# Kernel optimization log

Measured on AMD Instinct MI355X. Metric: run time of the kernel, lower is better.

The kernel has to match this reference:

```python
import jax, jax.numpy as jnp
import numpy as np

N, LQ, D_MODEL, M_HEADS, P_POINTS, H_DIM, W_DIM = 8, 4096, 256, 8, 4, 64, 64


def setup_inputs() -> dict:
    key = jax.random.key(0)
    ks = jax.random.split(key, 9)
    d = D_MODEL
    scale = 1.0 / np.sqrt(d).astype(np.float32)
    return {
        "query": jax.random.normal(ks[0], (N, LQ, d), jnp.float32),
        "reference_points": jax.random.uniform(ks[1], (N, LQ, 2), jnp.float32),
        "input_flatten": jax.random.normal(ks[2], (N, H_DIM * W_DIM, d), jnp.float32),
        "H": H_DIM,
        "W": W_DIM,
        "Wv": jax.random.normal(ks[3], (d, d), jnp.float32) * scale,
        "bv": jnp.zeros((d,), jnp.float32),
        "Woff": jax.random.normal(ks[4], (M_HEADS * P_POINTS * 2, d), jnp.float32) * 0.01,
        "boff": jax.random.normal(ks[5], (M_HEADS * P_POINTS * 2,), jnp.float32) * 0.5,
        "Wa": jax.random.normal(ks[6], (M_HEADS * P_POINTS, d), jnp.float32) * 0.01,
        "ba": jnp.zeros((M_HEADS * P_POINTS,), jnp.float32),
        "Wo": jax.random.normal(ks[7], (d, d), jnp.float32) * scale,
        "bo": jnp.zeros((d,), jnp.float32),
    }


def _bilinear_sample(val, grid, H, W):
    # val: [B, D, H*W]; grid: [B, Lq, P, 2] in [-1, 1] (x, y); align_corners=False, zero padding.
    B, D, _ = val.shape
    _, Lq, P, _ = grid.shape
    x = (grid[..., 0] + 1.0) * (W * 0.5) - 0.5
    y = (grid[..., 1] + 1.0) * (H * 0.5) - 0.5
    x0 = jnp.floor(x)
    y0 = jnp.floor(y)
    x0i = x0.astype(jnp.int32)
    y0i = y0.astype(jnp.int32)
    wx1 = x - x0
    wy1 = y - y0
    out = jnp.zeros((B, D, Lq, P), val.dtype)
    for xi, wx in ((x0i, 1.0 - wx1), (x0i + 1, wx1)):
        for yi, wy in ((y0i, 1.0 - wy1), (y0i + 1, wy1)):
            valid = (xi >= 0) & (xi < W) & (yi >= 0) & (yi < H)
            idx = jnp.clip(yi, 0, H - 1) * W + jnp.clip(xi, 0, W - 1)  # [B, Lq, P]
            g = jnp.take_along_axis(val, idx.reshape(B, 1, Lq * P), axis=2).reshape(B, D, Lq, P)
            w = jnp.where(valid, wx * wy, 0.0)
            out = out + g * w[:, None]
    return out


def reference(query, reference_points, input_flatten, H, W, Wv, bv, Woff, boff, Wa, ba, Wo, bo):
    n, lq, d = query.shape
    m, p = M_HEADS, P_POINTS
    dh = d // m
    value = (input_flatten @ Wv.T + bv).reshape(n, H * W, m, dh)
    offsets = (query @ Woff.T + boff).reshape(n, lq, m, p, 2)
    attw = jax.nn.softmax((query @ Wa.T + ba).reshape(n, lq, m, p), axis=-1)
    normalizer = jnp.array([W, H], dtype=query.dtype)  # [W, H] order per torch code
    loc = reference_points[:, :, None, None, :] + offsets / normalizer
    grid = 2.0 * loc - 1.0  # [n, lq, m, p, 2]
    # value -> [n*m, dh, H*W] matching torch flatten(2).transpose(1,2).reshape
    val = jnp.transpose(value, (0, 2, 3, 1)).reshape(n * m, dh, H * W)
    grd = jnp.transpose(grid, (0, 2, 1, 3, 4)).reshape(n * m, lq, p, 2)
    samp = _bilinear_sample(val, grd, H, W)  # [n*m, dh, lq, p]
    aw = jnp.transpose(attw, (0, 2, 1, 3)).reshape(n * m, 1, lq, p)
    out = (samp * aw).sum(-1).reshape(n, m * dh, lq)
    out = jnp.transpose(out, (0, 2, 1))  # [n, lq, d]
    return out @ Wo.T + bo
```

## Files before the change

### kernel.cpp

```cpp
#include <hip/hip_runtime.h>
#include <math.h>

#define NB   8
#define LQN  4096
#define DM   256
#define MH   8
#define PP   4
#define HH   64
#define WW   64
#define PW   67
#define PPIX (PW*PW)

typedef __bf16 bf16x8 __attribute__((ext_vector_type(8)));
typedef float  f32x4  __attribute__((ext_vector_type(4)));
typedef unsigned short us8 __attribute__((ext_vector_type(8)));
typedef unsigned short us4 __attribute__((ext_vector_type(4)));

__device__ __forceinline__ unsigned short f2bf(float f) {
    unsigned u = __float_as_uint(f);
    u += 0x7FFFu + ((u >> 16) & 1u);
    return (unsigned short)(u >> 16);
}
__device__ __forceinline__ float bf2f(unsigned short b) {
    return __uint_as_float((unsigned)b << 16);
}

__device__ __forceinline__ void gl2lds16(const void* g, unsigned short* l) {
    __builtin_amdgcn_global_load_lds(
        (const __attribute__((address_space(1))) void*)g,
        (__attribute__((address_space(3))) void*)l,
        16, 0, 0);
}

__device__ __forceinline__ bf16x8 cvt_frag(const unsigned short* s, int row, int kq) {
    const int u0 = row * 8 + ((kq * 2) ^ (row & 7));
    const int u1 = u0 ^ 1;
    const f32x4 a0 = *(const f32x4*)&s[u0 * 8];
    const f32x4 a1 = *(const f32x4*)&s[u1 * 8];
    bf16x8 v;
    v[0] = (__bf16)a0[0]; v[1] = (__bf16)a0[1];
    v[2] = (__bf16)a0[2]; v[3] = (__bf16)a0[3];
    v[4] = (__bf16)a1[0]; v[5] = (__bf16)a1[1];
    v[6] = (__bf16)a1[2]; v[7] = (__bf16)a1[3];
    return v;
}

__global__ __launch_bounds__(256)
void prep_kernel(const float* __restrict__ Wv, const float* __restrict__ Wo,
                 const float* __restrict__ Woff, const float* __restrict__ Wa,
                 const float* __restrict__ boff, const float* __restrict__ ba,
                 unsigned short* __restrict__ Wvh, unsigned short* __restrict__ Woh,
                 unsigned short* __restrict__ Wcath, float* __restrict__ bcat,
                 unsigned short* __restrict__ valueP) {
    const int i = blockIdx.x * 256 + threadIdx.x;
    if (i < 65536) {
        Wvh[i] = f2bf(Wv[i]);
    } else if (i < 131072) {
        const int j = i - 65536;
        Woh[j] = f2bf(Wo[j]);
    } else if (i < 163840) {
        const int j = i - 131072, n = j >> 8, k = j & 255;
        const float v = (n < 64) ? Woff[n * 256 + k]
                                 : ((n < 96) ? Wa[(n - 64) * 256 + k] : 0.f);
        Wcath[j] = f2bf(v);
    } else if (i < 163968) {
        const int n = i - 163840;
        bcat[n] = (n < 64) ? boff[n] : ((n < 96) ? ba[n - 64] : 0.f);
    } else if (i < 163968 + 201216) {
        const int j   = i - 163968;
        const int c4  = j & 63;
        const int pix = j >> 6;
        const int n   = pix / 393;
        const int r   = pix - n * 393;
        int x, y;
        if (r < 201) {
            const int q = r / 67;
            y = (q == 0) ? 0 : (q == 1 ? 65 : 66);
            x = r - q * 67;
        } else {
            const int q = r - 201;
            y = 1 + q / 3;
            const int s = q - (q / 3) * 3;
            x = (s == 0) ? 0 : (s == 1 ? 65 : 66);
        }
        const size_t addr = ((size_t)n * PPIX + (size_t)y * PW + x) * DM + c4 * 4;
        *(ushort4*)&valueP[addr] = make_ushort4(0, 0, 0, 0);
    }
}

__global__ __launch_bounds__(256, 4)
void value_gemm(const float* __restrict__ Ain,
                const unsigned short* __restrict__ Wvh,
                const float* __restrict__ bv,
                unsigned short* __restrict__ valueP) {
    constexpr int K = 256, NK = 8;
    __shared__ unsigned short sA[2][4096];
    __shared__ unsigned short sB[2][4096];

    const int t   = threadIdx.x;
    const int blk = blockIdx.x;
    const int xb  = blk & 7;
    const int idx = blk >> 3;
    const int brow = xb * 4096 + (idx >> 1) * 64;
    const int bcol = (idx & 1) * 128;

    const int srow = t >> 3;
    const int scq  = (t & 7) ^ (srow & 7);
    const float* aG = Ain + (size_t)(brow + srow) * K + scq * 4;
    const size_t aI = (size_t)32 * K;

    const unsigned short* bG = Wvh + (size_t)(bcol + (t >> 2)) * K + (t & 3) * 8;
    const size_t bI = (size_t)64 * K;

    const int l   = t & 63;
    const int wid = t >> 6;
    const int wr  = wid >> 1, wc = wid & 1;
    const int fr  = l & 15,   kq = l >> 4;

    f32x4 acc[2][4] = {};

#define STAGE(buf, ks_) { const int k0_ = (ks_) * 32;                    \
       gl2lds16(aG + k0_,      &sA[buf][t * 8]);                         \
       gl2lds16(aG + k0_ + aI, &sA[buf][2048 + t * 8]);                  \
       gl2lds16(bG + k0_,      &sB[buf][t * 8]);                         \
       gl2lds16(bG + k0_ + bI, &sB[buf][2048 + t * 8]); }

    STAGE(0, 0);
    STAGE(1, 1);

    for (int ks = 0; ks < NK; ++ks) {
        const int cur = ks & 1;
        if (ks < NK - 1) asm volatile("s_waitcnt vmcnt(4)" ::: "memory");
        else             asm volatile("s_waitcnt vmcnt(0)" ::: "memory");
        __builtin_amdgcn_s_barrier();
        __builtin_amdgcn_sched_barrier(0);

        bf16x8 af[2], bf_[4];
#pragma unroll
        for (int m = 0; m < 2; ++m)
            af[m]  = cvt_frag(sA[cur], wr * 32 + m * 16 + fr, kq);
#pragma unroll
        for (int n = 0; n < 4; ++n)
            bf_[n] = *(const bf16x8*)&sB[cur][(wc * 64 + n * 16 + fr) * 32 + kq * 8];

        __builtin_amdgcn_s_setprio(1);
#pragma unroll
        for (int m = 0; m < 2; ++m)
#pragma unroll
            for (int n = 0; n < 4; ++n)
                acc[m][n] = __builtin_amdgcn_mfma_f32_16x16x32_bf16(
                    bf_[n], af[m], acc[m][n], 0, 0, 0);
        __builtin_amdgcn_s_setprio(0);

        __builtin_amdgcn_sched_barrier(0);
        __builtin_amdgcn_s_barrier();
        if (ks + 2 < NK) STAGE(cur, ks + 2);
    }
#undef STAGE

#pragma unroll
    for (int m = 0; m < 2; ++m) {
        const int row = brow + wr * 32 + m * 16 + fr;
        const int nb_ = row >> 12;
        const int pix = row & 4095;
        const int y   = pix >> 6, x = pix & 63;
        const size_t rbase =
            ((size_t)nb_ * PPIX + (size_t)(y + 1) * PW + (x + 1)) * DM;
#pragma unroll
        for (int n = 0; n < 4; ++n) {
            const int colq = bcol + wc * 64 + n * 16 + kq * 4;
            const float4 b4 = *(const float4*)&bv[colq];
            us4 o;
            o[0] = f2bf(acc[m][n][0] + b4.x);
            o[1] = f2bf(acc[m][n][1] + b4.y);
            o[2] = f2bf(acc[m][n][2] + b4.z);
            o[3] = f2bf(acc[m][n][3] + b4.w);
            *(us4*)&valueP[rbase + colq] = o;
        }
    }
}

__global__ __launch_bounds__(512, 4)
void fused_lso(const float* __restrict__ query, const float* __restrict__ refp,
               const unsigned short* __restrict__ valueP,
               const unsigned short* __restrict__ Wcath,
               const float* __restrict__ bcat,
               const unsigned short* __restrict__ Woh,
               const float* __restrict__ bo, float* __restrict__ C) {
    constexpr int K = 256, NK = 8;
    extern __shared__ unsigned short smem[];
    unsigned short* sS = smem;
    unsigned short* sB = smem + 16384;
    unsigned short* sL = smem + 32768;

    const int t    = threadIdx.x;
    const int blk  = blockIdx.x;
    const int nb   = blk & 7;
    const int brow = nb * 4096 + (blk >> 3) * 64;
    const int w    = t >> 6;
    const int lane = t & 63;
    const int fr   = lane & 15, kq = lane >> 4;

    {
        unsigned short* sQ = sS;
        unsigned short* sW = sS + 8192;

        const int srow = t >> 3;
        const int scq  = (t & 7) ^ (srow & 7);
        const float* aG = query + (size_t)(brow + srow) * K + scq * 4;
        const unsigned short* wG = Wcath + (size_t)(t >> 2) * K + (t & 3) * 8;

        const int wr0 = w >> 2;
        const int wc0 = w & 3;

        f32x4 acc[2][2] = {};

#define STG0(buf, ks_) { const int k0_ = (ks_) * 32;                     \
       gl2lds16(aG + k0_, &sQ[(buf) * 4096 + t * 8]);                    \
       gl2lds16(wG + k0_, &sW[(buf) * 4096 + t * 8]); }

        STG0(0, 0);
        STG0(1, 1);

        for (int ks = 0; ks < NK; ++ks) {
            const int cur = ks & 1;
            if (ks < NK - 1) asm volatile("s_waitcnt vmcnt(2)" ::: "memory");
            else             asm volatile("s_waitcnt vmcnt(0)" ::: "memory");
            __builtin_amdgcn_s_barrier();
            __builtin_amdgcn_sched_barrier(0);

            bf16x8 af[2], bw[2];
#pragma unroll
            for (int m = 0; m < 2; ++m)
                af[m] = cvt_frag(&sQ[cur * 4096], wr0 * 32 + m * 16 + fr, kq);
#pragma unroll
            for (int n = 0; n < 2; ++n)
                bw[n] = *(const bf16x8*)&sW[cur * 4096 +
                        (wc0 * 32 + n * 16 + fr) * 32 + kq * 8];

            __builtin_amdgcn_s_setprio(1);
#pragma unroll
            for (int m = 0; m < 2; ++m)
#pragma unroll
                for (int n = 0; n < 2; ++n)
                    acc[m][n] = __builtin_amdgcn_mfma_f32_16x16x32_bf16(
                        bw[n], af[m], acc[m][n], 0, 0, 0);
            __builtin_amdgcn_s_setprio(0);

            __builtin_amdgcn_sched_barrier(0);
            __builtin_amdgcn_s_barrier();
            if (ks + 2 < NK) STG0(cur, ks + 2);
        }
#undef STG0

#pragma unroll
        for (int m = 0; m < 2; ++m) {
            const int row = wr0 * 32 + m * 16 + fr;
#pragma unroll
            for (int n = 0; n < 2; ++n) {
                const int colq = wc0 * 32 + n * 16 + kq * 4;
                const float4 b4 = *(const float4*)&bcat[colq];
                us4 o;
                o[0] = f2bf(acc[m][n][0] + b4.x);
                o[1] = f2bf(acc[m][n][1] + b4.y);
                o[2] = f2bf(acc[m][n][2] + b4.z);
                o[3] = f2bf(acc[m][n][3] + b4.w);
                *(us4*)&sL[row * 128 + colq] = o;
            }
        }
    }
    __syncthreads();

    {
        const int tp  = lane & 31;
        const int pm  = tp >> 2, ppt = tp & 3;
        const int half = lane >> 5;
        const int c8   = lane & 31;
        const int mh   = c8 >> 2;
        const unsigned short* vbase = valueP + (size_t)nb * (PPIX * DM) + c8 * 8;

        for (int i = 0; i < 8; i += 2) {
            const int qa = w * 8 + i;
            const int qb = qa + 1;

            us8 gA0[4], gB0[4]; float wA0[4], wB0[4];
            {
                const unsigned short* lg = sL + qa * 128;
                const int b = brow + qa;
                const float rx = refp[(size_t)b * 2 + 0];
                const float ry = refp[(size_t)b * 2 + 1];
                const float ox = bf2f(lg[pm * 8 + ppt * 2 + 0]);
                const float oy = bf2f(lg[pm * 8 + ppt * 2 + 1]);
                const float la = bf2f(lg[64 + tp]);
                const float x = fminf(fmaxf(fmaf(rx, (float)WW, ox) - 0.5f, -1.0f), 64.0f);
                const float y = fminf(fmaxf(fmaf(ry, (float)HH, oy) - 0.5f, -1.0f), 64.0f);
                float mx = fmaxf(la, __shfl_xor(la, 1));
                mx = fmaxf(mx, __shfl_xor(mx, 2));
                const float e = __expf(la - mx);
                float den = e + __shfl_xor(e, 1);
                den += __shfl_xor(den, 2);
                const float wgt = e / den;
#pragma unroll
                for (int p = 0; p < PP; ++p) {
                    const int   sl = mh * PP + p;
                    const float xp = __shfl(x, sl);
                    const float yp = __shfl(y, sl);
                    const float wp = __shfl(wgt, sl);
                    const float x0f = floorf(xp), y0f = floorf(yp);
                    const int   x0 = (int)x0f,   y0 = (int)y0f;
                    const float wx1 = xp - x0f,  wy1 = yp - y0f;
                    const float wy  = half ? wy1 : (1.f - wy1);
                    wA0[p] = wp * wy * (1.f - wx1);
                    wB0[p] = wp * wy * wx1;
                    const unsigned short* p0 =
                        vbase + (size_t)((y0 + 1 + half) * PW + (x0 + 1)) * DM;
                    gA0[p] = *(const us8*)(p0);
                    gB0[p] = *(const us8*)(p0 + DM);
                }
            }

            us8 gA1[4], gB1[4]; float wA1[4], wB1[4];
            {
                const unsigned short* lg = sL + qb * 128;
                const int b = brow + qb;
                const float rx = refp[(size_t)b * 2 + 0];
                const float ry = refp[(size_t)b * 2 + 1];
                const float ox = bf2f(lg[pm * 8 + ppt * 2 + 0]);
                const float oy = bf2f(lg[pm * 8 + ppt * 2 + 1]);
                const float la = bf2f(lg[64 + tp]);
                const float x = fminf(fmaxf(fmaf(rx, (float)WW, ox) - 0.5f, -1.0f), 64.0f);
                const float y = fminf(fmaxf(fmaf(ry, (float)HH, oy) - 0.5f, -1.0f), 64.0f);
                float mx = fmaxf(la, __shfl_xor(la, 1));
                mx = fmaxf(mx, __shfl_xor(mx, 2));
                const float e = __expf(la - mx);
                float den = e + __shfl_xor(e, 1);
                den += __shfl_xor(den, 2);
                const float wgt = e / den;
#pragma unroll
                for (int p = 0; p < PP; ++p) {
                    const int   sl = mh * PP + p;
                    const float xp = __shfl(x, sl);
                    const float yp = __shfl(y, sl);
                    const float wp = __shfl(wgt, sl);
                    const float x0f = floorf(xp), y0f = floorf(yp);
                    const int   x0 = (int)x0f,   y0 = (int)y0f;
                    const float wx1 = xp - x0f,  wy1 = yp - y0f;
                    const float wy  = half ? wy1 : (1.f - wy1);
                    wA1[p] = wp * wy * (1.f - wx1);
                    wB1[p] = wp * wy * wx1;
                    const unsigned short* p0 =
                        vbase + (size_t)((y0 + 1 + half) * PW + (x0 + 1)) * DM;
                    gA1[p] = *(const us8*)(p0);
                    gB1[p] = *(const us8*)(p0 + DM);
                }
            }

            {
                float accv[8] = {};
#pragma unroll
                for (int p = 0; p < PP; ++p)
#pragma unroll
                    for (int j = 0; j < 8; ++j) {
                        accv[j] = fmaf(wA0[p], bf2f(gA0[p][j]), accv[j]);
                        accv[j] = fmaf(wB0[p], bf2f(gB0[p][j]), accv[j]);
                    }
#pragma unroll
                for (int j = 0; j < 8; ++j)
                    accv[j] += __shfl_xor(accv[j], 32);
                if (half == 0) {
                    us8 o;
#pragma unroll
                    for (int j = 0; j < 8; ++j) o[j] = f2bf(accv[j]);
                    *(us8*)&sS[qa * 256 + ((c8 ^ (qa & 7)) * 8)] = o;
                }
            }
            {
                float accv[8] = {};
#pragma unroll
                for (int p = 0; p < PP; ++p)
#pragma unroll
                    for (int j = 0; j < 8; ++j) {
                        accv[j] = fmaf(wA1[p], bf2f(gA1[p][j]), accv[j]);
                        accv[j] = fmaf(wB1[p], bf2f(gB1[p][j]), accv[j]);
                    }
#pragma unroll
                for (int j = 0; j < 8; ++j)
                    accv[j] += __shfl_xor(accv[j], 32);
                if (half == 0) {
                    us8 o;
#pragma unroll
                    for (int j = 0; j < 8; ++j) o[j] = f2bf(accv[j]);
                    *(us8*)&sS[qb * 256 + ((c8 ^ (qb & 7)) * 8)] = o;
                }
            }
        }
    }
    __syncthreads();

    const unsigned short* bG = Woh + (size_t)(t >> 2) * K + (t & 3) * 8;
    const size_t rHalf = (size_t)128 * K;

    const int wr = w >> 2, wc = w & 3;

    f32x4 acc[2][4] = {};

#define STAGEF(buf, ks_) { const int k0_ = (ks_) * 32;                   \
       gl2lds16(bG + k0_,         &sB[(buf) * 8192 + t * 8]);            \
       gl2lds16(bG + k0_ + rHalf, &sB[(buf) * 8192 + 4096 + t * 8]); }

    STAGEF(0, 0);
    STAGEF(1, 1);

    for (int ks = 0; ks < NK; ++ks) {
        const int cur = ks & 1;
        if (ks < NK - 1) asm volatile("s_waitcnt vmcnt(2)" ::: "memory");
        else             asm volatile("s_waitcnt vmcnt(0)" ::: "memory");
        __builtin_amdgcn_s_barrier();
        __builtin_amdgcn_sched_barrier(0);

        bf16x8 af[2], bfr[4];
#pragma unroll
        for (int m = 0; m < 2; ++m) {
            const int row = wr * 32 + m * 16 + fr;
            const int u   = (ks * 4 + kq) ^ (row & 7);
            af[m] = *(const bf16x8*)&sS[row * 256 + u * 8];
        }
#pragma unroll
        for (int n = 0; n < 4; ++n)
            bfr[n] = *(const bf16x8*)&sB[cur * 8192 + (wc * 64 + n * 16 + fr) * 32 + kq * 8];

        __builtin_amdgcn_s_setprio(1);
#pragma unroll
        for (int m = 0; m < 2; ++m)
#pragma unroll
            for (int n = 0; n < 4; ++n)
                acc[m][n] = __builtin_amdgcn_mfma_f32_16x16x32_bf16(
                    bfr[n], af[m], acc[m][n], 0, 0, 0);
        __builtin_amdgcn_s_setprio(0);

        __builtin_amdgcn_sched_barrier(0);
        __builtin_amdgcn_s_barrier();
        if (ks + 2 < NK) STAGEF(cur, ks + 2);
    }
#undef STAGEF

#pragma unroll
    for (int m = 0; m < 2; ++m) {
        const int row = brow + wr * 32 + m * 16 + fr;
#pragma unroll
        for (int n = 0; n < 4; ++n) {
            const int colq = wc * 64 + n * 16 + kq * 4;
            const float4 bs = *(const float4*)&bo[colq];
            float4 o;
            o.x = acc[m][n][0] + bs.x; o.y = acc[m][n][1] + bs.y;
            o.z = acc[m][n][2] + bs.z; o.w = acc[m][n][3] + bs.w;
            *(float4*)&C[(size_t)row * DM + colq] = o;
        }
    }
}

extern "C" void kernel_launch(void* const* d_in, const int* in_sizes, int n_in,
                              void* d_out, int out_size, void* d_ws, size_t ws_size,
                              hipStream_t stream) {
    const float* query  = (const float*)d_in[0];
    const float* refp   = (const float*)d_in[1];
    const float* inputf = (const float*)d_in[2];
    const float* Wv   = (const float*)d_in[5];
    const float* bv   = (const float*)d_in[6];
    const float* Woff = (const float*)d_in[7];
    const float* boff = (const float*)d_in[8];
    const float* Wa   = (const float*)d_in[9];
    const float* ba   = (const float*)d_in[10];
    const float* Wo   = (const float*)d_in[11];
    const float* bo   = (const float*)d_in[12];
    float* out = (float*)d_out;

    unsigned short* valueP = (unsigned short*)d_ws;
    unsigned short* Wvh    = valueP + (size_t)NB * PPIX * DM;
    unsigned short* Woh    = Wvh    + 65536;
    unsigned short* Wcath  = Woh    + 65536;
    float*          bcat   = (float*)(Wcath + 32768);

    prep_kernel<<<1427, 256, 0, stream>>>(Wv, Wo, Woff, Wa, boff, ba,
                                          Wvh, Woh, Wcath, bcat, valueP);

    value_gemm<<<1024, 256, 0, stream>>>(inputf, Wvh, bv, valueP);

    fused_lso<<<512, 512, 81920, stream>>>(query, refp, valueP, Wcath, bcat,
                                           Woh, bo, out);
}
```

Baseline: 58.44 us.

## Halve fused block tile to 32 queries and split output GEMM into two passes

The fused sampling kernel now handles 32 query rows per block instead of 64, doubling the grid to 1024 blocks and halving shared memory to 40 KB. The output projection runs as two passes of 128 columns each, reusing one shared buffer so LDS stays small. The goal is more blocks resident per CU and a wider grid to hide gather latency. In exchange, every Wcath and Wo weight tile is reloaded twice as often, and each block does fewer MFMAs per barrier.

New measurement: 63.92 us. 9.4% more time.

```diff
diff --git a/kernel.cpp b/kernel.cpp
--- a/kernel.cpp
+++ b/kernel.cpp
@@ -190,33 +190,33 @@
     constexpr int K = 256, NK = 8;
     extern __shared__ unsigned short smem[];
     unsigned short* sS = smem;
-    unsigned short* sB = smem + 16384;
-    unsigned short* sL = smem + 32768;
+    unsigned short* sU = smem + 8192;
+    unsigned short* sL = smem + 16384;
 
     const int t    = threadIdx.x;
     const int blk  = blockIdx.x;
     const int nb   = blk & 7;
-    const int brow = nb * 4096 + (blk >> 3) * 64;
+    const int brow = nb * 4096 + (blk >> 3) * 32;
     const int w    = t >> 6;
     const int lane = t & 63;
     const int fr   = lane & 15, kq = lane >> 4;
 
     {
         unsigned short* sQ = sS;
-        unsigned short* sW = sS + 8192;
-
-        const int srow = t >> 3;
-        const int scq  = (t & 7) ^ (srow & 7);
-        const float* aG = query + (size_t)(brow + srow) * K + scq * 4;
+        unsigned short* sW = sU;
+
+        const int arow = t >> 3;
+        const int ascq = (t & 7) ^ (arow & 7);
+        const float* aG = query + (size_t)(brow + (arow & 31)) * K + ascq * 4;
         const unsigned short* wG = Wcath + (size_t)(t >> 2) * K + (t & 3) * 8;
 
         const int wr0 = w >> 2;
         const int wc0 = w & 3;
 
-        f32x4 acc[2][2] = {};
+        f32x4 acc[2] = {};
 
 #define STG0(buf, ks_) { const int k0_ = (ks_) * 32;                     \
-       gl2lds16(aG + k0_, &sQ[(buf) * 4096 + t * 8]);                    \
+       if (t < 256) gl2lds16(aG + k0_, &sQ[(buf) * 2048 + t * 8]);       \
        gl2lds16(wG + k0_, &sW[(buf) * 4096 + t * 8]); }
 
         STG0(0, 0);
@@ -224,15 +224,17 @@
 
         for (int ks = 0; ks < NK; ++ks) {
             const int cur = ks & 1;
-            if (ks < NK - 1) asm volatile("s_waitcnt vmcnt(2)" ::: "memory");
-            else             asm volatile("s_waitcnt vmcnt(0)" ::: "memory");
+            if (ks < NK - 1) {
+                if (w < 4) asm volatile("s_waitcnt vmcnt(2)" ::: "memory");
+                else       asm volatile("s_waitcnt vmcnt(1)" ::: "memory");
+            } else {
+                asm volatile("s_waitcnt vmcnt(0)" ::: "memory");
+            }
             __builtin_amdgcn_s_barrier();
             __builtin_amdgcn_sched_barrier(0);
 
-            bf16x8 af[2], bw[2];
-#pragma unroll
-            for (int m = 0; m < 2; ++m)
-                af[m] = cvt_frag(&sQ[cur * 4096], wr0 * 32 + m * 16 + fr, kq);
+            const bf16x8 af = cvt_frag(&sQ[cur * 2048], wr0 * 16 + fr, kq);
+            bf16x8 bw[2];
 #pragma unroll
             for (int n = 0; n < 2; ++n)
                 bw[n] = *(const bf16x8*)&sW[cur * 4096 +
@@ -240,11 +242,9 @@
 
             __builtin_amdgcn_s_setprio(1);
 #pragma unroll
-            for (int m = 0; m < 2; ++m)
-#pragma unroll
-                for (int n = 0; n < 2; ++n)
-                    acc[m][n] = __builtin_amdgcn_mfma_f32_16x16x32_bf16(
-                        bw[n], af[m], acc[m][n], 0, 0, 0);
+            for (int n = 0; n < 2; ++n)
+                acc[n] = __builtin_amdgcn_mfma_f32_16x16x32_bf16(
+                    bw[n], af, acc[n], 0, 0, 0);
             __builtin_amdgcn_s_setprio(0);
 
             __builtin_amdgcn_sched_barrier(0);
@@ -253,20 +253,17 @@
         }
 #undef STG0
 
-#pragma unroll
-        for (int m = 0; m < 2; ++m) {
-            const int row = wr0 * 32 + m * 16 + fr;
-#pragma unroll
-            for (int n = 0; n < 2; ++n) {
-                const int colq = wc0 * 32 + n * 16 + kq * 4;
-                const float4 b4 = *(const float4*)&bcat[colq];
-                us4 o;
-                o[0] = f2bf(acc[m][n][0] + b4.x);
-                o[1] = f2bf(acc[m][n][1] + b4.y);
-                o[2] = f2bf(acc[m][n][2] + b4.z);
-                o[3] = f2bf(acc[m][n][3] + b4.w);
-                *(us4*)&sL[row * 128 + colq] = o;
-            }
+        const int row = wr0 * 16 + fr;
+#pragma unroll
+        for (int n = 0; n < 2; ++n) {
+            const int colq = wc0 * 32 + n * 16 + kq * 4;
+            const float4 b4 = *(const float4*)&bcat[colq];
+            us4 o;
+            o[0] = f2bf(acc[n][0] + b4.x);
+            o[1] = f2bf(acc[n][1] + b4.y);
+            o[2] = f2bf(acc[n][2] + b4.z);
+            o[3] = f2bf(acc[n][3] + b4.w);
+            *(us4*)&sL[row * 128 + colq] = o;
         }
     }
     __syncthreads();
@@ -279,8 +276,8 @@
         const int mh   = c8 >> 2;
         const unsigned short* vbase = valueP + (size_t)nb * (PPIX * DM) + c8 * 8;
 
-        for (int i = 0; i < 8; i += 2) {
-            const int qa = w * 8 + i;
+        for (int i = 0; i < 4; i += 2) {
+            const int qa = w * 4 + i;
             const int qb = qa + 1;
 
             us8 gA0[4], gB0[4]; float wA0[4], wB0[4];
@@ -397,64 +394,56 @@
     }
     __syncthreads();
 
-    const unsigned short* bG = Woh + (size_t)(t >> 2) * K + (t & 3) * 8;
-    const size_t rHalf = (size_t)128 * K;
-
     const int wr = w >> 2, wc = w & 3;
-
-    f32x4 acc[2][4] = {};
-
-#define STAGEF(buf, ks_) { const int k0_ = (ks_) * 32;                   \
-       gl2lds16(bG + k0_,         &sB[(buf) * 8192 + t * 8]);            \
-       gl2lds16(bG + k0_ + rHalf, &sB[(buf) * 8192 + 4096 + t * 8]); }
-
-    STAGEF(0, 0);
-    STAGEF(1, 1);
-
-    for (int ks = 0; ks < NK; ++ks) {
-        const int cur = ks & 1;
-        if (ks < NK - 1) asm volatile("s_waitcnt vmcnt(2)" ::: "memory");
-        else             asm volatile("s_waitcnt vmcnt(0)" ::: "memory");
-        __builtin_amdgcn_s_barrier();
-        __builtin_amdgcn_sched_barrier(0);
-
-        bf16x8 af[2], bfr[4];
-#pragma unroll
-        for (int m = 0; m < 2; ++m) {
-            const int row = wr * 32 + m * 16 + fr;
-            const int u   = (ks * 4 + kq) ^ (row & 7);
-            af[m] = *(const bf16x8*)&sS[row * 256 + u * 8];
-        }
-#pragma unroll
-        for (int n = 0; n < 4; ++n)
-            bfr[n] = *(const bf16x8*)&sB[cur * 8192 + (wc * 64 + n * 16 + fr) * 32 + kq * 8];
-
-        __builtin_amdgcn_s_setprio(1);
-#pragma unroll
-        for (int m = 0; m < 2; ++m)
-#pragma unroll
-            for (int n = 0; n < 4; ++n)
-                acc[m][n] = __builtin_amdgcn_mfma_f32_16x16x32_bf16(
-                    bfr[n], af[m], acc[m][n], 0, 0, 0);
-        __builtin_amdgcn_s_setprio(0);
-
-        __builtin_amdgcn_sched_barrier(0);
-        __builtin_amdgcn_s_barrier();
-        if (ks + 2 < NK) STAGEF(cur, ks + 2);
-    }
-#undef STAGEF
-
-#pragma unroll
-    for (int m = 0; m < 2; ++m) {
-        const int row = brow + wr * 32 + m * 16 + fr;
-#pragma unroll
-        for (int n = 0; n < 4; ++n) {
-            const int colq = wc * 64 + n * 16 + kq * 4;
+#pragma unroll
+    for (int pass = 0; pass < 2; ++pass) {
+        const unsigned short* bG =
+            Woh + (size_t)(pass * 128 + (t >> 2)) * K + (t & 3) * 8;
+        f32x4 acc2[2] = {};
+
+#define STAGEP(buf, ks_) gl2lds16(bG + (ks_) * 32, &sU[(buf) * 4096 + t * 8]);
+
+        STAGEP(0, 0);
+        STAGEP(1, 1);
+
+        for (int ks = 0; ks < NK; ++ks) {
+            const int cur = ks & 1;
+            if (ks < NK - 1) asm volatile("s_waitcnt vmcnt(1)" ::: "memory");
+            else             asm volatile("s_waitcnt vmcnt(0)" ::: "memory");
+            __builtin_amdgcn_s_barrier();
+            __builtin_amdgcn_sched_barrier(0);
+
+            const int row = wr * 16 + fr;
+            const bf16x8 af =
+                *(const bf16x8*)&sS[row * 256 + (((ks * 4 + kq) ^ (row & 7)) * 8)];
+            bf16x8 bfr[2];
+#pragma unroll
+            for (int n = 0; n < 2; ++n)
+                bfr[n] = *(const bf16x8*)&sU[cur * 4096 +
+                         (wc * 32 + n * 16 + fr) * 32 + kq * 8];
+
+            __builtin_amdgcn_s_setprio(1);
+#pragma unroll
+            for (int n = 0; n < 2; ++n)
+                acc2[n] = __builtin_amdgcn_mfma_f32_16x16x32_bf16(
+                    bfr[n], af, acc2[n], 0, 0, 0);
+            __builtin_amdgcn_s_setprio(0);
+
+            __builtin_amdgcn_sched_barrier(0);
+            __builtin_amdgcn_s_barrier();
+            if (ks + 2 < NK) STAGEP(cur, ks + 2);
+        }
+#undef STAGEP
+
+        const int grow = brow + wr * 16 + fr;
+#pragma unroll
+        for (int n = 0; n < 2; ++n) {
+            const int colq = pass * 128 + wc * 32 + n * 16 + kq * 4;
             const float4 bs = *(const float4*)&bo[colq];
             float4 o;
-            o.x = acc[m][n][0] + bs.x; o.y = acc[m][n][1] + bs.y;
-            o.z = acc[m][n][2] + bs.z; o.w = acc[m][n][3] + bs.w;
-            *(float4*)&C[(size_t)row * DM + colq] = o;
+            o.x = acc2[n][0] + bs.x; o.y = acc2[n][1] + bs.y;
+            o.z = acc2[n][2] + bs.z; o.w = acc2[n][3] + bs.w;
+            *(float4*)&C[(size_t)grow * DM + colq] = o;
         }
     }
 }
@@ -486,6 +475,6 @@
 
     value_gemm<<<1024, 256, 0, stream>>>(inputf, Wvh, bv, valueP);
 
-    fused_lso<<<512, 512, 81920, stream>>>(query, refp, valueP, Wcath, bcat,
-                                           Woh, bo, out);
-}
+    fused_lso<<<1024, 512, 40960, stream>>>(query, refp, valueP, Wcath, bcat,
+                                            Woh, bo, out);
+}
```
